# Kernel optimization log

Hardware: AMD Instinct MI355X
Metric: run time of the kernel (lower is better)

Reference implementation:

```python
import jax, jax.numpy as jnp
import numpy as np
from jax import lax

B, C_IN, T, H, W_SP = 4, 16, 31, 128, 128
HID = 16


def setup_inputs() -> dict:
    key = jax.random.key(0)
    k1, k2 = jax.random.split(key)
    x = jax.random.normal(k1, (B, C_IN, T, H, W_SP), dtype=jnp.float32)
    # Conv3d weight: (out=2*hidden, in, kD, kH, kW), Kaiming-ish scale
    Wt = jax.random.normal(k2, (2 * HID, C_IN, 3, 3, 3), dtype=jnp.float32) * (1.0 / np.sqrt(C_IN * 27))
    b = jnp.zeros((2 * HID,), dtype=jnp.float32)
    return {"x": x, "W": Wt, "b": b}


def reference(x, W, b):
    # 3D conv producing gates: [B, 2*HID, T, H, W]
    gates = lax.conv_general_dilated(
        x, W, window_strides=(1, 1, 1), padding="SAME",
        dimension_numbers=("NCDHW", "OIDHW", "NCDHW"),
    ) + b[None, :, None, None, None]
    Z = jnp.tanh(gates[:, :HID])          # candidate, [B, HID, T, H, W]
    F = jax.nn.sigmoid(gates[:, HID:])    # forget gate

    # fo-pool recurrence over time: h_t = f_t * h_{t-1} + (1 - f_t) * z_t
    Zt = jnp.moveaxis(Z, 2, 0)  # [T, B, HID, H, W]
    Ft = jnp.moveaxis(F, 2, 0)

    def step(h, zf):
        z, f = zf
        h_new = f * h + (1.0 - f) * z
        return h_new, h_new

    h0 = jnp.zeros((B, HID, H, W_SP), dtype=x.dtype)  # state=None -> h starts at 0
    _, hs = lax.scan(step, h0, (Zt, Ft))
    return jnp.moveaxis(hs, 0, 2)  # [B, HID, T, H, W]
```

## Files before the change

### kernel.cpp

```cpp
#include <hip/hip_runtime.h>
#include <hip/hip_bf16.h>
#include <math.h>


namespace {
constexpr int kB = 4, kC = 16, kT = 31, kH = 128, kW = 128, kHid = 16;
constexpr int kHW  = kH * kW;
constexpr int kTHW = kT * kHW;
constexpr int kCS  = 16;
constexpr int kRS  = 130 * kCS;
constexpr int kPS  = 3 * kRS;
constexpr int kSlots = 4;
}

typedef __attribute__((ext_vector_type(8)))  short  short8;
typedef __attribute__((ext_vector_type(16))) float  floatx16;

__device__ __forceinline__ unsigned short f2bf(float f) {
    __hip_bfloat16 h = __float2bfloat16(f);
    return __builtin_bit_cast(unsigned short, h);
}

__device__ __forceinline__ void stage_plane(
    unsigned short* __restrict__ lds, const float* __restrict__ xb,
    int t_, int h, int tid)
{
    const int slot = (t_ + 2 * kSlots) & (kSlots - 1);
    unsigned short* pl = lds + slot * kPS;
    const int w  = tid & 127;
    const int c0 = (tid >> 7) * 8;
    const int wp = w + 1;
    const int sw = c0 ^ ((wp & 1) * 8);
    const bool tvalid = (t_ >= 0 && t_ < kT);
#pragma unroll
    for (int kh = 0; kh < 3; ++kh) {
        const int hr = h + kh - 1;
        short8 v = {0, 0, 0, 0, 0, 0, 0, 0};
        if (tvalid && hr >= 0 && hr < kH) {
            const float* src = xb + c0 * kTHW + t_ * kHW + hr * kW + w;
            float f[8];
#pragma unroll
            for (int j = 0; j < 8; ++j) f[j] = src[j * kTHW];
#pragma unroll
            for (int j = 0; j < 8; ++j) v[j] = (short)f2bf(f[j]);
        }
        *(short8*)(pl + kh * kRS + wp * kCS + sw) = v;
    }
}

__global__ __launch_bounds__(256, 2) void qrnn_mfma(
    const float* __restrict__ x, const float* __restrict__ Wt,
    const float* __restrict__ bias, float* __restrict__ out)
{
    __shared__ unsigned short lds[kSlots * kPS];

    const int id  = blockIdx.x;
    const int bh  = (id & 7) * 64 + (id >> 3);
    const int b   = bh >> 7;
    const int h   = bh & (kH - 1);

    const int tid  = threadIdx.x;
    const int lane = tid & 63;
    const int m    = lane & 31;
    const int hi   = lane >> 5;
    const int chi  = hi * 8;
    const int n0   = (tid >> 6) * 32;

    const float* xb = x + b * (kC * kTHW);

    short8 wf[27];
#pragma unroll
    for (int tap = 0; tap < 27; ++tap) {
        short8 v;
#pragma unroll
        for (int j = 0; j < 8; ++j)
            v[j] = (short)f2bf(Wt[m * (kC * 27) + (chi + j) * 27 + tap]);
        wf[tap] = v;
    }

    float st[8], zb[8], fbv[8];
    int ooff[8];
    const int P = n0 + m;
#pragma unroll
    for (int r = 0; r < 8; ++r) {
        const int hid = (r & 3) + 8 * (r >> 2) + 4 * hi;
        zb[r]  = bias[hid];
        fbv[r] = bias[kHid + hid];
        st[r]  = 0.0f;
        ooff[r] = ((b * kHid + hid) * kT) * kHW + h * kW + P;
    }

    unsigned short* bA = lds + P * kCS       + (chi ^ ((P & 1) * 8));
    unsigned short* bB = lds + (P + 1) * kCS + (chi ^ (((P + 1) & 1) * 8));

    stage_plane(lds, xb, -1, h, tid);
    stage_plane(lds, xb,  0, h, tid);
    if (tid < 48) {
        const int s = tid / 12, rem = tid % 12;
        const int row = rem >> 2, q = rem & 3;
        const int wp = (q & 1) * 129;
        const int c0 = (q >> 1) * 8;
        const short8 z = {0, 0, 0, 0, 0, 0, 0, 0};
        *(short8*)(lds + s * kPS + row * kRS + wp * kCS + (c0 ^ ((wp & 1) * 8))) = z;
    }

    for (int t = 0; t < kT; ++t) {
        stage_plane(lds, xb, t + 1, h, tid);
        __syncthreads();

        floatx16 acc = {0,0,0,0,0,0,0,0,0,0,0,0,0,0,0,0};
#pragma unroll
        for (int kd = 0; kd < 3; ++kd) {
            const int soff = ((t + kd + 2 * kSlots - 1) & (kSlots - 1)) * kPS;
#pragma unroll
            for (int kh = 0; kh < 3; ++kh) {
                const int o = soff + kh * kRS;
                const short8 b0 = *(const short8*)(bA + o);
                const short8 b1 = *(const short8*)(bB + o);
                const short8 b2 = *(const short8*)(bA + o + 2 * kCS);
                acc = __builtin_amdgcn_mfma_f32_32x32x16_bf16(wf[kd*9 + kh*3 + 0], b0, acc, 0, 0, 0);
                acc = __builtin_amdgcn_mfma_f32_32x32x16_bf16(wf[kd*9 + kh*3 + 1], b1, acc, 0, 0, 0);
                acc = __builtin_amdgcn_mfma_f32_32x32x16_bf16(wf[kd*9 + kh*3 + 2], b2, acc, 0, 0, 0);
            }
        }

#pragma unroll
        for (int r = 0; r < 8; ++r) {
            const float zp = acc[r]     + zb[r];
            const float fp = acc[r + 8] + fbv[r];
            const float e2 = __expf(2.0f * zp);
            const float z  = 1.0f - 2.0f * __builtin_amdgcn_rcpf(e2 + 1.0f);
            const float f  = __builtin_amdgcn_rcpf(1.0f + __expf(-fp));
            st[r] = z + f * (st[r] - z);
            out[ooff[r] + t * kHW] = st[r];
        }
    }
}

extern "C" void kernel_launch(void* const* d_in, const int* in_sizes, int n_in,
                              void* d_out, int out_size, void* d_ws, size_t ws_size,
                              hipStream_t stream) {
    const float* x    = (const float*)d_in[0];
    const float* Wt   = (const float*)d_in[1];
    const float* bias = (const float*)d_in[2];
    float* out = (float*)d_out;

    qrnn_mfma<<<dim3(kB * kH), dim3(256), 0, stream>>>(x, Wt, bias, out);
}
```

Before: 286.7 us.

## Prefetch next input plane into registers with float4 loads during MFMA compute

Replaces the synchronous per-step plane staging with a split issue/commit scheme. Global loads for plane t+2 are issued into registers right after the barrier, so they overlap the MFMA work, and are written to LDS as bf16 at the start of the next step. Loads are widened to float4 per thread, using 192 threads instead of 256. This adds 32 live VGPRs for the prefetch buffer, which may pressure occupancy under the 2-blocks launch bound.

```diff
diff --git a/kernel.cpp b/kernel.cpp
--- a/kernel.cpp
+++ b/kernel.cpp
@@ -14,38 +14,12 @@
 }
 
 typedef __attribute__((ext_vector_type(8)))  short  short8;
+typedef __attribute__((ext_vector_type(4)))  float  floatv4;
 typedef __attribute__((ext_vector_type(16))) float  floatx16;
 
 __device__ __forceinline__ unsigned short f2bf(float f) {
     __hip_bfloat16 h = __float2bfloat16(f);
     return __builtin_bit_cast(unsigned short, h);
-}
-
-__device__ __forceinline__ void stage_plane(
-    unsigned short* __restrict__ lds, const float* __restrict__ xb,
-    int t_, int h, int tid)
-{
-    const int slot = (t_ + 2 * kSlots) & (kSlots - 1);
-    unsigned short* pl = lds + slot * kPS;
-    const int w  = tid & 127;
-    const int c0 = (tid >> 7) * 8;
-    const int wp = w + 1;
-    const int sw = c0 ^ ((wp & 1) * 8);
-    const bool tvalid = (t_ >= 0 && t_ < kT);
-#pragma unroll
-    for (int kh = 0; kh < 3; ++kh) {
-        const int hr = h + kh - 1;
-        short8 v = {0, 0, 0, 0, 0, 0, 0, 0};
-        if (tvalid && hr >= 0 && hr < kH) {
-            const float* src = xb + c0 * kTHW + t_ * kHW + hr * kW + w;
-            float f[8];
-#pragma unroll
-            for (int j = 0; j < 8; ++j) f[j] = src[j * kTHW];
-#pragma unroll
-            for (int j = 0; j < 8; ++j) v[j] = (short)f2bf(f[j]);
-        }
-        *(short8*)(pl + kh * kRS + wp * kCS + sw) = v;
-    }
 }
 
 __global__ __launch_bounds__(256, 2) void qrnn_mfma(
@@ -93,8 +67,41 @@
     unsigned short* bA = lds + P * kCS       + (chi ^ ((P & 1) * 8));
     unsigned short* bB = lds + (P + 1) * kCS + (chi ^ (((P + 1) & 1) * 8));
 
-    stage_plane(lds, xb, -1, h, tid);
-    stage_plane(lds, xb,  0, h, tid);
+    const bool sact = tid < 192;
+    const int  skh  = tid >> 6;
+    const int  swq  = tid & 31;
+    const int  soct = (tid >> 5) & 1;
+    const int  shr  = h + skh - 1;
+    const bool srow = sact && (shr >= 0) && (shr < kH);
+    const float* sbase = xb + (soct * 8) * kTHW + shr * kW + swq * 4;
+    unsigned short* cb0 = lds + skh * kRS + (swq * 4 + 1) * kCS;
+
+    floatv4 sv[8];
+
+    auto sissue = [&](int tp) {
+#pragma unroll
+        for (int j = 0; j < 8; ++j) sv[j] = floatv4{0.f, 0.f, 0.f, 0.f};
+        if (srow && (unsigned)tp < (unsigned)kT) {
+            const float* s = sbase + tp * kHW;
+#pragma unroll
+            for (int j = 0; j < 8; ++j)
+                sv[j] = *(const floatv4*)(s + j * kTHW);
+        }
+    };
+    auto scommit = [&](int tp) {
+        if (sact) {
+            unsigned short* pl = cb0 + ((tp + 2 * kSlots) & (kSlots - 1)) * kPS;
+#pragma unroll
+            for (int q = 0; q < 4; ++q) {
+                const int sw = (soct * 8) ^ ((((q + 1) & 1)) * 8);
+                short8 v;
+#pragma unroll
+                for (int j = 0; j < 8; ++j) v[j] = (short)f2bf(sv[j][q]);
+                *(short8*)(pl + q * kCS + sw) = v;
+            }
+        }
+    };
+
     if (tid < 48) {
         const int s = tid / 12, rem = tid % 12;
         const int row = rem >> 2, q = rem & 3;
@@ -104,9 +111,14 @@
         *(short8*)(lds + s * kPS + row * kRS + wp * kCS + (c0 ^ ((wp & 1) * 8))) = z;
     }
 
+    sissue(-1); scommit(-1);
+    sissue(0);  scommit(0);
+    sissue(1);
+
     for (int t = 0; t < kT; ++t) {
-        stage_plane(lds, xb, t + 1, h, tid);
+        scommit(t + 1);
         __syncthreads();
+        sissue(t + 2);
 
         floatx16 acc = {0,0,0,0,0,0,0,0,0,0,0,0,0,0,0,0};
 #pragma unroll
```

After: 260.2 us. 1.1x faster.
